# Performance work log

Measured on AMD Instinct MI355X. Metric: run time of the kernel, lower is better.

## Reference

```python
import jax, jax.numpy as jnp
import numpy as np

BIG_NEG = -1.0e6  # constants.big_negative


def setup_inputs() -> dict:
    key = jax.random.key(0)
    ks = jax.random.split(key, 10)
    B, N, NF, HNF, M, T = 2048, 100, 128, 128, 128, 12
    hidden_output_nodes = jax.random.normal(ks[0], (B, N, HNF), dtype=jnp.float32)
    input_nodes = jax.random.normal(ks[1], (B, N, NF), dtype=jnp.float32)
    node_mask = jax.random.uniform(ks[2], (B, N)) < 0.8
    node_mask = node_mask.at[:, 0].set(True)  # avoid fully-masked rows
    s = 0.05
    W_emb = jax.random.normal(ks[3], (M, NF + HNF), dtype=jnp.float32) * s
    b_emb = jnp.zeros((M,), dtype=jnp.float32)
    W_ih = jax.random.normal(ks[4], (4 * M, M), dtype=jnp.float32) * s
    b_ih = jnp.zeros((4 * M,), dtype=jnp.float32)
    W_hh = jax.random.normal(ks[5], (4 * M, M), dtype=jnp.float32) * s
    b_hh = jnp.zeros((4 * M,), dtype=jnp.float32)
    return {
        "hidden_output_nodes": hidden_output_nodes,
        "input_nodes": input_nodes,
        "W_emb": W_emb, "b_emb": b_emb,
        "W_ih": W_ih, "b_ih": b_ih, "W_hh": W_hh, "b_hh": b_hh,
        "node_mask": node_mask,
        "lstm_computations": T,
    }


def _set2vec(hidden_output_nodes, input_nodes, W_emb, b_emb, W_ih, b_ih, W_hh, b_hh, node_mask, T):
    B = input_nodes.shape[0]
    M = W_emb.shape[0]
    # memory: [B, N, M]
    cat = jnp.concatenate((hidden_output_nodes, input_nodes), axis=2)
    memory = jnp.einsum("bnf,mf->bnm", cat, W_emb) + b_emb
    energy_mask = (~node_mask).astype(memory.dtype) * BIG_NEG  # [B, N]

    zeros = jnp.zeros((B, M), dtype=memory.dtype)

    def step(carry, _):
        lstm_in, h, c = carry
        # LSTMCell (PyTorch gate order: i, f, g, o)
        gates = lstm_in @ W_ih.T + b_ih + h @ W_hh.T + b_hh
        i, f, g, o = jnp.split(gates, 4, axis=-1)
        c = jax.nn.sigmoid(f) * c + jax.nn.sigmoid(i) * jnp.tanh(g)
        q = jax.nn.sigmoid(o) * jnp.tanh(c)  # query / new hidden state
        # dot-product attention read over the node memory
        energies = jnp.einsum("bm,bnm->bn", q, memory) + energy_mask
        attn = jax.nn.softmax(energies, axis=1)
        read = jnp.einsum("bn,bnm->bm", attn, memory)
        return (read, q, c), None

    (read, q, _), _ = jax.lax.scan(step, (zeros, zeros, zeros), None, length=T)
    return jnp.concatenate((q, read), axis=1)  # [B, 2*M]


def reference(hidden_output_nodes, input_nodes, W_emb, b_emb, W_ih, b_ih, W_hh, b_hh, node_mask, lstm_computations):
    return _set2vec(hidden_output_nodes, input_nodes, W_emb, b_emb, W_ih, b_ih, W_hh, b_hh, node_mask, lstm_computations)
```

## Files before the change

### kernel.cpp

```cpp
#include <hip/hip_runtime.h>
#include <hip/hip_fp16.h>
#include <math.h>

#define BIG_NEG  (-1.0e6f)
#define NN   100
#define MD   128
#define KD   256
#define G4   512
#define NB   4
#define MP2  68
#define XPAD 288

#define WS_WGF_H  32768
#define WS_BIAS_F 81920

typedef _Float16 f16x2 __attribute__((ext_vector_type(2)));
typedef _Float16 f16x8 __attribute__((ext_vector_type(8)));
typedef float    f32x4 __attribute__((ext_vector_type(4)));

__device__ __forceinline__ float sigm(float x) { return 1.0f / (1.0f + __expf(-x)); }

extern "C" __global__ void prep_kernel(const float* __restrict__ W_emb,
                                       const float* __restrict__ W_ih,
                                       const float* __restrict__ b_ih,
                                       const float* __restrict__ W_hh,
                                       const float* __restrict__ b_hh,
                                       float* __restrict__ ws) {
    int tid = blockIdx.x * blockDim.x + threadIdx.x;
    int nth = gridDim.x * blockDim.x;
    __half* WF    = (__half*)ws;
    __half* WG    = (__half*)ws + WS_WGF_H;
    float*  biasc = ws + WS_BIAS_F;
    for (int i = tid; i < 32768; i += nth) {
        int kg = i >> 10, m = (i >> 3) & 127, j = i & 7;
        WF[i] = __float2half(W_emb[m * 256 + kg * 8 + j]);
    }
    for (int i = tid; i < 131072; i += nth) {
        int kc = i >> 12, g = (i >> 3) & 511, j = i & 7;
        int k = kc * 8 + j;
        float w = (k < 128) ? W_ih[g * 128 + k] : W_hh[g * 128 + (k - 128)];
        WG[i] = __float2half(w);
    }
    for (int i = tid; i < 512; i += nth) biasc[i] = b_ih[i] + b_hh[i];
}

extern "C" __global__ __launch_bounds__(1024, 4)
void set2vec_main(const float* __restrict__ hidden,
                  const float* __restrict__ input,
                  const float* __restrict__ b_emb,
                  const unsigned char* __restrict__ mask_bytes,
                  const int* __restrict__ Tptr,
                  const float* __restrict__ ws,
                  float* __restrict__ out) {
    __shared__ __half2 mem2[NB][NN][MP2];
    __shared__ __half  xcath[NB][XPAD];
    __shared__ float   xcat2[NB][KD];
    __shared__ float   cbuf[NB][MD];
    __shared__ float   emask[NB][NN];
    __shared__ float   bbuf[G4];
    __shared__ int     mask_is_u8;
    __shared__ float   gbuf[NB][G4];
    __shared__ float   epart[NB][NN][2];
    __shared__ float   abuf[NB][NN];

    const int tid  = threadIdx.x;
    const int b0   = blockIdx.x * NB;
    const int lane = tid & 63, wv = tid >> 6;
    const int ln15 = lane & 15, lhi = lane >> 4;
    const __half* WF = (const __half*)ws;

    if (tid == 0) {
        int nz = 0;
        for (int i = 0; i < 64; ++i)
            if ((i & 3) && mask_bytes[i]) nz = 1;
        mask_is_u8 = nz;
    }

    {
        const float be0 = b_emb[0 * 16 + ln15], be1 = b_emb[1 * 16 + ln15];
        const float be2 = b_emb[2 * 16 + ln15], be3 = b_emb[3 * 16 + ln15];
        const float be4 = b_emb[4 * 16 + ln15], be5 = b_emb[5 * 16 + ln15];
        const float be6 = b_emb[6 * 16 + ln15], be7 = b_emb[7 * 16 + ln15];
        __half* memh = (__half*)mem2;
        for (int tile = wv; tile < 25; tile += 16) {
            f32x4 acc0 = {be0, be0, be0, be0}, acc1 = {be1, be1, be1, be1};
            f32x4 acc2 = {be2, be2, be2, be2}, acc3 = {be3, be3, be3, be3};
            f32x4 acc4 = {be4, be4, be4, be4}, acc5 = {be5, be5, be5, be5};
            f32x4 acc6 = {be6, be6, be6, be6}, acc7 = {be7, be7, be7, be7};

            const int rA     = tile * 16 + ln15;
            const int rAok   = rA < NB * NN;
            const long gbase = ((long)(b0 * NN + rA)) << 7;

            #pragma unroll 1
            for (int mk = 0; mk < 8; ++mk) {
                f16x8 aF;
                if (rAok) {
                    int k0 = mk * 32 + lhi * 8;
                    const float* src = (k0 < 128) ? (hidden + gbase + k0)
                                                  : (input + gbase + (k0 - 128));
                    float4 v0 = *(const float4*)src;
                    float4 v1 = *(const float4*)(src + 4);
                    union { f16x8 v; f16x2 h[4]; } au;
                    au.h[0] = __builtin_bit_cast(f16x2, __builtin_amdgcn_cvt_pkrtz(v0.x, v0.y));
                    au.h[1] = __builtin_bit_cast(f16x2, __builtin_amdgcn_cvt_pkrtz(v0.z, v0.w));
                    au.h[2] = __builtin_bit_cast(f16x2, __builtin_amdgcn_cvt_pkrtz(v1.x, v1.y));
                    au.h[3] = __builtin_bit_cast(f16x2, __builtin_amdgcn_cvt_pkrtz(v1.z, v1.w));
                    aF = au.v;
                } else {
                    aF = (f16x8)(_Float16)0.0f;
                }
                const __half* wrow = WF + ((mk * 4 + lhi) * 128 + ln15) * 8;
#define EMB_CT(CT, ACC) { \
                union { uint4 u; f16x8 v; } bu; \
                bu.u = *(const uint4*)(wrow + (CT * 16) * 8); \
                ACC = __builtin_amdgcn_mfma_f32_16x16x32_f16(aF, bu.v, ACC, 0, 0, 0); }
                EMB_CT(0, acc0) EMB_CT(1, acc1) EMB_CT(2, acc2) EMB_CT(3, acc3)
                EMB_CT(4, acc4) EMB_CT(5, acc5) EMB_CT(6, acc6) EMB_CT(7, acc7)
#undef EMB_CT
            }
#define EMB_WR(CT, ACC) { \
            _Pragma("unroll") \
            for (int reg = 0; reg < 4; ++reg) { \
                int r = tile * 16 + lhi * 4 + reg; \
                if (r < NB * NN) { \
                    int bb = r / NN, n = r - (r / NN) * NN; \
                    memh[(bb * NN + n) * (2 * MP2) + CT * 16 + ln15] = __float2half(ACC[reg]); \
                } } }
            EMB_WR(0, acc0) EMB_WR(1, acc1) EMB_WR(2, acc2) EMB_WR(3, acc3)
            EMB_WR(4, acc4) EMB_WR(5, acc5) EMB_WR(6, acc6) EMB_WR(7, acc7)
#undef EMB_WR
        }
    }

    const uint4* WgB = (const uint4*)((const __half*)ws + WS_WGF_H);
    const int ct0 = wv * 2, ct1 = wv * 2 + 1;
#define LDW(KS) \
    const uint4 wA##KS = WgB[((KS) * 4 + lhi) * 512 + ct0 * 16 + ln15]; \
    const uint4 wB##KS = WgB[((KS) * 4 + lhi) * 512 + ct1 * 16 + ln15];
    LDW(0) LDW(1) LDW(2) LDW(3) LDW(4) LDW(5) LDW(6) LDW(7)
#undef LDW

    for (int i = tid; i < NB * XPAD; i += 1024) ((__half*)xcath)[i] = __float2half(0.0f);
    ((float*)xcat2)[tid] = 0.0f;
    if (tid < NB * MD) ((float*)cbuf)[tid] = 0.0f;
    if (tid < G4) bbuf[tid] = ws[WS_BIAS_F + tid];
    if (tid < NB * NN) {
        int bb = tid / NN, n = tid - bb * NN;
        long mrow = (long)(b0 + bb) * NN + n;
        int valid = mask_is_u8 ? (mask_bytes[mrow] != 0)
                               : (((const int*)mask_bytes)[mrow] != 0);
        emask[bb][n] = valid ? 0.0f : BIG_NEG;
    }
    __syncthreads();

    const int T = Tptr[0];

    const __half* aBase = &xcath[ln15 & 3][lhi * 8];

    const int e_act = tid < 800;
    const int e_bb  = tid / 200;
    const int e_r   = tid - e_bb * 200;
    const int e_n   = e_r >> 1;
    const int e_mh  = e_r & 1;

    for (int step = 0; step < T; ++step) {
        {
            f32x4 ga = {0.f, 0.f, 0.f, 0.f}, gb = {0.f, 0.f, 0.f, 0.f};
#define GS(KS) { \
            union { uint4 u; f16x8 v; } a, ba, bc; \
            a.u  = *(const uint4*)(aBase + (KS) * 32); \
            ba.u = wA##KS; bc.u = wB##KS; \
            ga = __builtin_amdgcn_mfma_f32_16x16x32_f16(a.v, ba.v, ga, 0, 0, 0); \
            gb = __builtin_amdgcn_mfma_f32_16x16x32_f16(a.v, bc.v, gb, 0, 0, 0); }
            GS(0) GS(1) GS(2) GS(3) GS(4) GS(5) GS(6) GS(7)
#undef GS
            if (lhi == 0) {
                #pragma unroll
                for (int r = 0; r < 4; ++r) {
                    gbuf[r][ct0 * 16 + ln15] = ga[r];
                    gbuf[r][ct1 * 16 + ln15] = gb[r];
                }
            }
        }
        __syncthreads();
        if (tid < NB * MD) {
            int bb = tid >> 7, m = tid & 127;
            float gi = gbuf[bb][m]       + bbuf[m];
            float gf = gbuf[bb][128 + m] + bbuf[128 + m];
            float gg = gbuf[bb][256 + m] + bbuf[256 + m];
            float go = gbuf[bb][384 + m] + bbuf[384 + m];
            float c  = cbuf[bb][m];
            c = sigm(gf) * c + sigm(gi) * tanhf(gg);
            float qv = sigm(go) * tanhf(c);
            cbuf[bb][m] = c;
            xcat2[bb][128 + m] = qv;
            xcath[bb][128 + m] = __float2half(qv);
        }
        __syncthreads();
        if (e_act) {
            const uint4*  mr4 = (const uint4*)&mem2[e_bb][e_n][e_mh * 32];
            const float4* qv4 = (const float4*)&xcat2[e_bb][128 + e_mh * 64];
            float e = 0.0f;
            #pragma unroll
            for (int i = 0; i < 8; ++i) {
                uint4  mu = mr4[i];
                float4 qa = qv4[2 * i], qb = qv4[2 * i + 1];
                float2 m0 = __half22float2(*(__half2*)&mu.x);
                float2 m1 = __half22float2(*(__half2*)&mu.y);
                float2 m2 = __half22float2(*(__half2*)&mu.z);
                float2 m3 = __half22float2(*(__half2*)&mu.w);
                e = fmaf(qa.x, m0.x, e); e = fmaf(qa.y, m0.y, e);
                e = fmaf(qa.z, m1.x, e); e = fmaf(qa.w, m1.y, e);
                e = fmaf(qb.x, m2.x, e); e = fmaf(qb.y, m2.y, e);
                e = fmaf(qb.z, m3.x, e); e = fmaf(qb.w, m3.y, e);
            }
            epart[e_bb][e_n][e_mh] = e;
        }
        __syncthreads();
        if (tid < 256) {
            int bb = tid >> 6, l = tid & 63;
            float e0 = epart[bb][l][0] + epart[bb][l][1] + emask[bb][l];
            float e1 = -INFINITY;
            if (l < 36) {
                int n1 = l + 64;
                e1 = epart[bb][n1][0] + epart[bb][n1][1] + emask[bb][n1];
            }
            float mx = fmaxf(e0, e1);
            for (int off = 32; off; off >>= 1) mx = fmaxf(mx, __shfl_xor(mx, off, 64));
            float p0 = __expf(e0 - mx);
            float p1 = (l < 36) ? __expf(e1 - mx) : 0.0f;
            float s = p0 + p1;
            for (int off = 32; off; off >>= 1) s += __shfl_xor(s, off, 64);
            float inv = 1.0f / s;
            abuf[bb][l] = p0 * inv;
            if (l < 36) abuf[bb][l + 64] = p1 * inv;
        }
        __syncthreads();
        if (tid < 256) {
            int bb = tid >> 6, mp = tid & 63;
            const float*   ar  = abuf[bb];
            const __half2* mrp = &mem2[bb][0][mp];
            float r0 = 0, r1 = 0, r2 = 0, r3 = 0, s0 = 0, s1 = 0, s2 = 0, s3 = 0;
            #pragma unroll 5
            for (int n = 0; n < 100; n += 4) {
                float4  av = *(const float4*)(ar + n);
                __half2 h0 = mrp[n * MP2],       h1 = mrp[(n + 1) * MP2];
                __half2 h2 = mrp[(n + 2) * MP2], h3 = mrp[(n + 3) * MP2];
                float2 f0 = __half22float2(h0), f1 = __half22float2(h1);
                float2 f2 = __half22float2(h2), f3 = __half22float2(h3);
                r0 = fmaf(av.x, f0.x, r0); s0 = fmaf(av.x, f0.y, s0);
                r1 = fmaf(av.y, f1.x, r1); s1 = fmaf(av.y, f1.y, s1);
                r2 = fmaf(av.z, f2.x, r2); s2 = fmaf(av.z, f2.y, s2);
                r3 = fmaf(av.w, f3.x, r3); s3 = fmaf(av.w, f3.y, s3);
            }
            float rx = (r0 + r1) + (r2 + r3);
            float ry = (s0 + s1) + (s2 + s3);
            int m = mp * 2;
            xcat2[bb][m]     = rx;
            xcat2[bb][m + 1] = ry;
            xcath[bb][m]     = __float2half(rx);
            xcath[bb][m + 1] = __float2half(ry);
        }
        __syncthreads();
    }

    {
        int bb = tid >> 8, j = tid & 255;
        float v = (j < 128) ? xcat2[bb][128 + j] : xcat2[bb][j - 128];
        out[((long)(b0 + bb) << 8) + j] = v;
    }
}

extern "C" void kernel_launch(void* const* d_in, const int* in_sizes, int n_in,
                              void* d_out, int out_size, void* d_ws, size_t ws_size,
                              hipStream_t stream) {
    const float* hidden = (const float*)d_in[0];
    const float* input  = (const float*)d_in[1];
    const float* W_emb  = (const float*)d_in[2];
    const float* b_emb  = (const float*)d_in[3];
    const float* W_ih   = (const float*)d_in[4];
    const float* b_ih   = (const float*)d_in[5];
    const float* W_hh   = (const float*)d_in[6];
    const float* b_hh   = (const float*)d_in[7];
    const unsigned char* mask = (const unsigned char*)d_in[8];
    const int*  Tptr    = (const int*)d_in[9];
    float* ws   = (float*)d_ws;
    float* outp = (float*)d_out;

    hipLaunchKernelGGL(prep_kernel, dim3(128), dim3(256), 0, stream,
                       W_emb, W_ih, b_ih, W_hh, b_hh, ws);
    hipLaunchKernelGGL(set2vec_main, dim3(512), dim3(1024), 0, stream,
                       hidden, input, b_emb, mask, Tptr, ws, outp);
}
```

Before: 185.1 us.

## Compute attention energies with MFMA and restructure the attention read for vector LDS loads

Replaces the scalar per-thread energy dot products with f16 MFMA tiles over the node memory, using the f16 query copy as the A operand. The attention read loop now has each lane load 8 halves per node over a quarter of the nodes, followed by a cross-lane shuffle reduction and vectorized stores. Sigmoid and tanh switch to fast reciprocal and clamped exp forms. The aim is to cut per-step VALU and LDS latency in the serial 12-step recurrence, at the cost of f16 rounding of the query in the energies and approximate transcendentals.

```diff
diff --git a/kernel.cpp b/kernel.cpp
--- a/kernel.cpp
+++ b/kernel.cpp
@@ -18,7 +18,22 @@
 typedef _Float16 f16x8 __attribute__((ext_vector_type(8)));
 typedef float    f32x4 __attribute__((ext_vector_type(4)));
 
-__device__ __forceinline__ float sigm(float x) { return 1.0f / (1.0f + __expf(-x)); }
+#if __has_builtin(__builtin_amdgcn_rcpf)
+#define RCPF(x) __builtin_amdgcn_rcpf(x)
+#else
+#define RCPF(x) (1.0f / (x))
+#endif
+
+#define PKRTZ(a, b) __builtin_bit_cast(unsigned, __builtin_amdgcn_cvt_pkrtz((a), (b)))
+
+__device__ __forceinline__ float sigm(float x) {
+    return RCPF(1.0f + __expf(-x));
+}
+__device__ __forceinline__ float tanh_f(float x) {
+    float xc = fminf(fmaxf(x, -15.0f), 15.0f);
+    float e  = __expf(2.0f * xc);
+    return (e - 1.0f) * RCPF(e + 1.0f);
+}
 
 extern "C" __global__ void prep_kernel(const float* __restrict__ W_emb,
                                        const float* __restrict__ W_ih,
@@ -60,14 +75,15 @@
     __shared__ float   bbuf[G4];
     __shared__ int     mask_is_u8;
     __shared__ float   gbuf[NB][G4];
-    __shared__ float   epart[NB][NN][2];
+    __shared__ float   ebuf[NB][128];
     __shared__ float   abuf[NB][NN];
 
     const int tid  = threadIdx.x;
     const int b0   = blockIdx.x * NB;
     const int lane = tid & 63, wv = tid >> 6;
     const int ln15 = lane & 15, lhi = lane >> 4;
-    const __half* WF = (const __half*)ws;
+    const __half* WF   = (const __half*)ws;
+    const __half* memh = (const __half*)mem2;
 
     if (tid == 0) {
         int nz = 0;
@@ -81,7 +97,7 @@
         const float be2 = b_emb[2 * 16 + ln15], be3 = b_emb[3 * 16 + ln15];
         const float be4 = b_emb[4 * 16 + ln15], be5 = b_emb[5 * 16 + ln15];
         const float be6 = b_emb[6 * 16 + ln15], be7 = b_emb[7 * 16 + ln15];
-        __half* memh = (__half*)mem2;
+        __half* memw = (__half*)mem2;
         for (int tile = wv; tile < 25; tile += 16) {
             f32x4 acc0 = {be0, be0, be0, be0}, acc1 = {be1, be1, be1, be1};
             f32x4 acc2 = {be2, be2, be2, be2}, acc3 = {be3, be3, be3, be3};
@@ -101,11 +117,11 @@
                                                   : (input + gbase + (k0 - 128));
                     float4 v0 = *(const float4*)src;
                     float4 v1 = *(const float4*)(src + 4);
-                    union { f16x8 v; f16x2 h[4]; } au;
-                    au.h[0] = __builtin_bit_cast(f16x2, __builtin_amdgcn_cvt_pkrtz(v0.x, v0.y));
-                    au.h[1] = __builtin_bit_cast(f16x2, __builtin_amdgcn_cvt_pkrtz(v0.z, v0.w));
-                    au.h[2] = __builtin_bit_cast(f16x2, __builtin_amdgcn_cvt_pkrtz(v1.x, v1.y));
-                    au.h[3] = __builtin_bit_cast(f16x2, __builtin_amdgcn_cvt_pkrtz(v1.z, v1.w));
+                    union { f16x8 v; unsigned u[4]; } au;
+                    au.u[0] = PKRTZ(v0.x, v0.y);
+                    au.u[1] = PKRTZ(v0.z, v0.w);
+                    au.u[2] = PKRTZ(v1.x, v1.y);
+                    au.u[3] = PKRTZ(v1.z, v1.w);
                     aF = au.v;
                 } else {
                     aF = (f16x8)(_Float16)0.0f;
@@ -125,7 +141,7 @@
                 int r = tile * 16 + lhi * 4 + reg; \
                 if (r < NB * NN) { \
                     int bb = r / NN, n = r - (r / NN) * NN; \
-                    memh[(bb * NN + n) * (2 * MP2) + CT * 16 + ln15] = __float2half(ACC[reg]); \
+                    memw[(bb * NN + n) * (2 * MP2) + CT * 16 + ln15] = __float2half(ACC[reg]); \
                 } } }
             EMB_WR(0, acc0) EMB_WR(1, acc1) EMB_WR(2, acc2) EMB_WR(3, acc3)
             EMB_WR(4, acc4) EMB_WR(5, acc5) EMB_WR(6, acc6) EMB_WR(7, acc7)
@@ -158,11 +174,19 @@
 
     const __half* aBase = &xcath[ln15 & 3][lhi * 8];
 
-    const int e_act = tid < 800;
-    const int e_bb  = tid / 200;
-    const int e_r   = tid - e_bb * 200;
-    const int e_n   = e_r >> 1;
-    const int e_mh  = e_r & 1;
+    const int ep0 = wv * 2, ep1 = wv * 2 + 1;
+    const int e_bb0 = ep0 / 7, e_nt0 = ep0 - e_bb0 * 7;
+    const int e_bb1 = ep1 / 7, e_nt1 = ep1 - e_bb1 * 7;
+    const int e_n0  = e_nt0 * 16 + ln15, e_n1 = e_nt1 * 16 + ln15;
+    const int e_n0c = (e_n0 < 100) ? e_n0 : 99;
+    const int e_n1c = (e_n1 < 100) ? e_n1 : 99;
+    const __half* eB0 = memh + (e_bb0 * NN + e_n0c) * (2 * MP2) + lhi * 8;
+    const __half* eB1 = memh + (e_bb1 * NN + e_n1c) * (2 * MP2) + lhi * 8;
+    const __half* eA0 = &xcath[e_bb0][128 + lhi * 8];
+    const __half* eA1 = &xcath[e_bb1][128 + lhi * 8];
+
+    const int r_s = lane >> 2, r_nq = lane & 3;
+    const __half* rBase = memh + (wv & 3) * NN * (2 * MP2) + r_s * 8;
 
     for (int step = 0; step < T; ++step) {
         {
@@ -191,76 +215,80 @@
             float gg = gbuf[bb][256 + m] + bbuf[256 + m];
             float go = gbuf[bb][384 + m] + bbuf[384 + m];
             float c  = cbuf[bb][m];
-            c = sigm(gf) * c + sigm(gi) * tanhf(gg);
-            float qv = sigm(go) * tanhf(c);
+            c = sigm(gf) * c + sigm(gi) * tanh_f(gg);
+            float qv = sigm(go) * tanh_f(c);
             cbuf[bb][m] = c;
             xcat2[bb][128 + m] = qv;
             xcath[bb][128 + m] = __float2half(qv);
         }
         __syncthreads();
-        if (e_act) {
-            const uint4*  mr4 = (const uint4*)&mem2[e_bb][e_n][e_mh * 32];
-            const float4* qv4 = (const float4*)&xcat2[e_bb][128 + e_mh * 64];
-            float e = 0.0f;
-            #pragma unroll
-            for (int i = 0; i < 8; ++i) {
-                uint4  mu = mr4[i];
-                float4 qa = qv4[2 * i], qb = qv4[2 * i + 1];
-                float2 m0 = __half22float2(*(__half2*)&mu.x);
-                float2 m1 = __half22float2(*(__half2*)&mu.y);
-                float2 m2 = __half22float2(*(__half2*)&mu.z);
-                float2 m3 = __half22float2(*(__half2*)&mu.w);
-                e = fmaf(qa.x, m0.x, e); e = fmaf(qa.y, m0.y, e);
-                e = fmaf(qa.z, m1.x, e); e = fmaf(qa.w, m1.y, e);
-                e = fmaf(qb.x, m2.x, e); e = fmaf(qb.y, m2.y, e);
-                e = fmaf(qb.z, m3.x, e); e = fmaf(qb.w, m3.y, e);
-            }
-            epart[e_bb][e_n][e_mh] = e;
+        if (wv < 14) {
+            f32x4 e0 = {0.f, 0.f, 0.f, 0.f}, e1 = {0.f, 0.f, 0.f, 0.f};
+#define ES(KS) { \
+            union { uint4 u; f16x8 v; } a0, a1, bq0, bq1; \
+            a0.u  = *(const uint4*)(eA0 + (KS) * 32); \
+            bq0.u = *(const uint4*)(eB0 + (KS) * 32); \
+            a1.u  = *(const uint4*)(eA1 + (KS) * 32); \
+            bq1.u = *(const uint4*)(eB1 + (KS) * 32); \
+            e0 = __builtin_amdgcn_mfma_f32_16x16x32_f16(a0.v, bq0.v, e0, 0, 0, 0); \
+            e1 = __builtin_amdgcn_mfma_f32_16x16x32_f16(a1.v, bq1.v, e1, 0, 0, 0); }
+            ES(0) ES(1) ES(2) ES(3)
+#undef ES
+            if (lhi == 0) {
+                if (e_n0 < 100) ebuf[e_bb0][e_n0] = e0[0];
+                if (e_n1 < 100) ebuf[e_bb1][e_n1] = e1[0];
+            }
         }
         __syncthreads();
         if (tid < 256) {
             int bb = tid >> 6, l = tid & 63;
-            float e0 = epart[bb][l][0] + epart[bb][l][1] + emask[bb][l];
+            float e0 = ebuf[bb][l] + emask[bb][l];
             float e1 = -INFINITY;
-            if (l < 36) {
-                int n1 = l + 64;
-                e1 = epart[bb][n1][0] + epart[bb][n1][1] + emask[bb][n1];
-            }
+            if (l < 36) e1 = ebuf[bb][l + 64] + emask[bb][l + 64];
             float mx = fmaxf(e0, e1);
             for (int off = 32; off; off >>= 1) mx = fmaxf(mx, __shfl_xor(mx, off, 64));
             float p0 = __expf(e0 - mx);
             float p1 = (l < 36) ? __expf(e1 - mx) : 0.0f;
             float s = p0 + p1;
             for (int off = 32; off; off >>= 1) s += __shfl_xor(s, off, 64);
-            float inv = 1.0f / s;
+            float inv = RCPF(s);
             abuf[bb][l] = p0 * inv;
             if (l < 36) abuf[bb][l + 64] = p1 * inv;
         }
         __syncthreads();
         if (tid < 256) {
-            int bb = tid >> 6, mp = tid & 63;
-            const float*   ar  = abuf[bb];
-            const __half2* mrp = &mem2[bb][0][mp];
-            float r0 = 0, r1 = 0, r2 = 0, r3 = 0, s0 = 0, s1 = 0, s2 = 0, s3 = 0;
+            int bb = wv & 3;
+            float a0 = 0.f, a1 = 0.f, a2 = 0.f, a3 = 0.f;
+            float a4 = 0.f, a5 = 0.f, a6 = 0.f, a7 = 0.f;
             #pragma unroll 5
-            for (int n = 0; n < 100; n += 4) {
-                float4  av = *(const float4*)(ar + n);
-                __half2 h0 = mrp[n * MP2],       h1 = mrp[(n + 1) * MP2];
-                __half2 h2 = mrp[(n + 2) * MP2], h3 = mrp[(n + 3) * MP2];
-                float2 f0 = __half22float2(h0), f1 = __half22float2(h1);
-                float2 f2 = __half22float2(h2), f3 = __half22float2(h3);
-                r0 = fmaf(av.x, f0.x, r0); s0 = fmaf(av.x, f0.y, s0);
-                r1 = fmaf(av.y, f1.x, r1); s1 = fmaf(av.y, f1.y, s1);
-                r2 = fmaf(av.z, f2.x, r2); s2 = fmaf(av.z, f2.y, s2);
-                r3 = fmaf(av.w, f3.x, r3); s3 = fmaf(av.w, f3.y, s3);
-            }
-            float rx = (r0 + r1) + (r2 + r3);
-            float ry = (s0 + s1) + (s2 + s3);
-            int m = mp * 2;
-            xcat2[bb][m]     = rx;
-            xcat2[bb][m + 1] = ry;
-            xcath[bb][m]     = __float2half(rx);
-            xcath[bb][m + 1] = __float2half(ry);
+            for (int j = 0; j < 25; ++j) {
+                int n = r_nq * 25 + j;
+                float av = abuf[bb][n];
+                uint4 u  = *(const uint4*)(rBase + n * (2 * MP2));
+                float2 f0 = __half22float2(*(__half2*)&u.x);
+                float2 f1 = __half22float2(*(__half2*)&u.y);
+                float2 f2 = __half22float2(*(__half2*)&u.z);
+                float2 f3 = __half22float2(*(__half2*)&u.w);
+                a0 = fmaf(av, f0.x, a0); a1 = fmaf(av, f0.y, a1);
+                a2 = fmaf(av, f1.x, a2); a3 = fmaf(av, f1.y, a3);
+                a4 = fmaf(av, f2.x, a4); a5 = fmaf(av, f2.y, a5);
+                a6 = fmaf(av, f3.x, a6); a7 = fmaf(av, f3.y, a7);
+            }
+#define RED(A) A += __shfl_xor(A, 1, 64); A += __shfl_xor(A, 2, 64);
+            RED(a0) RED(a1) RED(a2) RED(a3) RED(a4) RED(a5) RED(a6) RED(a7)
+#undef RED
+            if (r_nq == 0) {
+                int m = r_s * 8;
+                float4 lo = {a0, a1, a2, a3}, hi = {a4, a5, a6, a7};
+                *(float4*)&xcat2[bb][m]     = lo;
+                *(float4*)&xcat2[bb][m + 4] = hi;
+                uint4 hv;
+                hv.x = PKRTZ(a0, a1);
+                hv.y = PKRTZ(a2, a3);
+                hv.z = PKRTZ(a4, a5);
+                hv.w = PKRTZ(a6, a7);
+                *(uint4*)&xcath[bb][m] = hv;
+            }
         }
         __syncthreads();
     }
```

Measured after the change: 171.9 us. 7.1% less time.
